# Optimization experiments

Hardware: AMD Instinct MI355X
Metric: run time of the kernel (lower is better)

Reference implementation:

```python
import jax, jax.numpy as jnp
import numpy as np

# SMPL-like kinematic tree parents for 21 body joints (child j -> parent index in the 22-slot feature)
KTREE_PARENTS = jnp.array([0, 0, 0, 1, 2, 3, 4, 5, 6, 7, 8, 9, 9, 9, 12, 13, 14, 16, 17, 18, 19], dtype=jnp.int32)
# np.linspace(22, 64, 3, endpoint=False, dtype=int)[::-1] for num_tokens=64, token_size_div=3, num_joints+1=22
UP_SIZES = [50, 36, 22]
NUM_JOINTS_P1 = 22


def conv1d_rep(x, w, b):
    # x: (B, Cin, L), w: (Cout, Cin, 3), replicate padding of 1 on each side
    xp = jnp.pad(x, ((0, 0), (0, 0), (1, 1)), mode='edge')
    y = jax.lax.conv_general_dilated(xp, w, (1,), 'VALID', dimension_numbers=('NCH', 'OIH', 'NCH'))
    return y + b[None, :, None]


def interp_linear(x, out_size):
    # torch nn.Upsample(mode='linear', align_corners=False) semantics; x: (B, C, L)
    L = x.shape[-1]
    coords = (jnp.arange(out_size, dtype=x.dtype) + 0.5) * (L / out_size) - 0.5
    coords = jnp.clip(coords, 0.0, L - 1)
    lo = jnp.floor(coords).astype(jnp.int32)
    hi = jnp.minimum(lo + 1, L - 1)
    w = coords - lo.astype(x.dtype)
    return x[..., lo] * (1.0 - w) + x[..., hi] * w


def rotation_6d_to_matrix(d6):
    # pytorch3d convention: rows b1, b2, b3 stacked at dim=-2
    a1, a2 = d6[..., :3], d6[..., 3:]
    b1 = a1 / jnp.linalg.norm(a1, axis=-1, keepdims=True)
    a2p = a2 - jnp.sum(b1 * a2, axis=-1, keepdims=True) * b1
    b2 = a2p / jnp.linalg.norm(a2p, axis=-1, keepdims=True)
    b3 = jnp.cross(b1, b2)
    return jnp.stack([b1, b2, b3], axis=-2)


def setup_inputs() -> dict:
    key = jax.random.key(0)
    ks = jax.random.split(key, 8)
    B, T, C, W, J, D = 1024, 64, 512, 512, 21, 6
    s = 0.02
    f32 = jnp.float32
    return {
        'x': jax.random.normal(ks[0], (B, T, C), f32),
        'conv1_w': jax.random.normal(ks[1], (W, C, 3), f32) * s,
        'conv1_b': jnp.zeros((W,), f32),
        'tok_w': jax.random.normal(ks[2], (T, T), f32) * s,
        'tok_b': jnp.zeros((T,), f32),
        'up_w': jax.random.normal(ks[3], (3, W, W, 3), f32) * s,
        'up_b': jnp.zeros((3, W), f32),
        'ln_g': jnp.ones((W,), f32),
        'ln_b': jnp.zeros((W,), f32),
        'beta_w': jax.random.normal(ks[4], (W, 10), f32) * s,
        'beta_b': jnp.zeros((10,), f32),
        'pw1': jax.random.normal(ks[5], (J, 2 * W, W), f32) * s,
        'pb1': jnp.zeros((J, W), f32),
        'pw2': jax.random.normal(ks[6], (J, W, D), f32) * s,
        'pb2': jax.random.normal(ks[7], (J, D), f32) * 0.1,
    }


def reference(x, conv1_w, conv1_b, tok_w, tok_b, up_w, up_b, ln_g, ln_b,
              beta_w, beta_b, pw1, pb1, pw2, pb2):
    # ---- decoder ----
    h = x.transpose(0, 2, 1)                                   # (B, C, T)
    h = jax.nn.relu(conv1d_rep(h, conv1_w, conv1_b))            # (B, W, T)
    # Conv1d(T, T, 1) applied on token axis (after permutes) == matmul over tokens
    h = jax.nn.relu(jnp.einsum('st,bwt->bws', tok_w, h) + tok_b[None, None, :])  # (B, W, T)
    for i, sz in enumerate(UP_SIZES):
        h = conv1d_rep(interp_linear(h, sz), up_w[i], up_b[i])
        if sz != NUM_JOINTS_P1:
            h = jax.nn.relu(h)
    # h: (B, W, 22)
    m = h.mean(axis=-1)                                         # (B, W)
    mu = m.mean(-1, keepdims=True)
    var = m.var(-1, keepdims=True)
    pred_beta = ((m - mu) / jnp.sqrt(var + 1e-5) * ln_g + ln_b) @ beta_w + beta_b  # (B, 10)
    jf = h.transpose(0, 2, 1)                                   # (B, 22, W)
    curr = jf[:, 1:, :]                                         # joint j+1 feats, (B, 21, W)
    parent = jf[:, KTREE_PARENTS, :]                            # parent feats,   (B, 21, W)
    feat = jnp.concatenate([curr, parent], axis=-1)             # (B, 21, 2W)
    hid = jax.nn.relu(jnp.einsum('bjc,jch->bjh', feat, pw1) + pb1[None])
    pose6d = jnp.einsum('bjh,jhd->bjd', hid, pw2) + pb2[None]   # (B, 21, 6)
    rotmat = rotation_6d_to_matrix(pose6d)                      # (B, 21, 3, 3)
    return pose6d, rotmat, pred_beta
```

## Files before the change

### kernel.cpp

```cpp
#include <hip/hip_runtime.h>


typedef unsigned short u16;
typedef unsigned short u16x4 __attribute__((ext_vector_type(4)));
typedef unsigned short u16x8 __attribute__((ext_vector_type(8)));
typedef float f32x4 __attribute__((ext_vector_type(4)));
typedef __bf16 bf16x8 __attribute__((ext_vector_type(8)));

__constant__ int KPAR_C[21] = {0,0,0,1,2,3,4,5,6,7,8,9,9,9,12,13,14,16,17,18,19};

__device__ __forceinline__ u16 bf16rne(float v) {
  unsigned b = __builtin_bit_cast(unsigned, v);
  return (u16)((b + 0x7fffu + ((b >> 16) & 1u)) >> 16);
}
__device__ __forceinline__ float bf16tof(u16 h) {
  unsigned b = ((unsigned)h) << 16;
  return __builtin_bit_cast(float, b);
}
__device__ __forceinline__ f32x4 mfma16(u16x8 a, u16x8 b, f32x4 c) {
  return __builtin_amdgcn_mfma_f32_16x16x32_bf16(
      __builtin_bit_cast(bf16x8, a), __builtin_bit_cast(bf16x8, b), c, 0, 0, 0);
}
__device__ __forceinline__ int unpack_c(int p) {
  return (p & ~31) | (((p >> 3) & 3) << 2) | (p & 3) | ((p & 4) << 2);
}
__device__ __forceinline__ void gload_lds16(const void* g, void* l) {
  __builtin_amdgcn_global_load_lds((const __attribute__((address_space(1))) void*)g,
                                   (__attribute__((address_space(3))) void*)l, 16, 0, 0);
}

__global__ __launch_bounds__(256)
void kwprep(const float* __restrict__ conv1_w, const float* __restrict__ up_w,
            const float* __restrict__ tok_w, u16* __restrict__ WF, u16* __restrict__ TWF) {
  int idx = blockIdx.x * 256 + threadIdx.x;
  if (idx < 786432) {
    const int lane = idx & 63;
    int r = idx >> 6;
    const int nf = r & 15; r >>= 4;
    const int ks = r % 48; r /= 48;
    const int p = r & 1; r >>= 1;
    const int nh = r & 1;
    const int L = r >> 1;
    const float* Wsrc = (L == 0) ? conv1_w : (up_w + (size_t)(L - 1) * 786432);
    const int wcol = unpack_c(nh * 256 + nf * 16 + (lane & 15));
    u16x8 o;
#pragma unroll
    for (int e = 0; e < 8; ++e) {
      const int k = ks * 32 + ((lane >> 4) << 2) + (e & 3) + ((e >> 2) << 4);
      const int c = k & 511, kk = k >> 9;
      const float v = Wsrc[(size_t)wcol * 1536 + c * 3 + kk];
      const u16 h = bf16rne(v);
      o[e] = p ? bf16rne(v - bf16tof(h)) : h;
    }
    *(u16x8*)(WF + (size_t)idx * 8) = o;
  } else if (idx < 786432 + 1024) {
    const int i2 = idx - 786432;
    const int lane = i2 & 63;
    const int r = i2 >> 6;
    const int mf = r & 3;
    const int ks = (r >> 2) & 1;
    const int p = r >> 3;
    const int s = mf * 16 + (lane & 15);
    u16x8 o;
#pragma unroll
    for (int e = 0; e < 8; ++e) {
      const int t = ks * 32 + ((lane >> 4) << 2) + (e & 3) + ((e >> 2) << 4);
      const float v = tok_w[s * 64 + t];
      const u16 h = bf16rne(v);
      o[e] = p ? bf16rne(v - bf16tof(h)) : h;
    }
    *(u16x8*)(TWF + (size_t)i2 * 8) = o;
  }
}

__global__ __launch_bounds__(256)
void kpw1prep(const float* __restrict__ pw1, u16* __restrict__ PWF) {
  const int idx = blockIdx.x * 256 + threadIdx.x;
  if (idx >= 2752512) return;
  const int lane = idx & 63;
  const int nf = (idx >> 6) & 15;
  const int ks = (idx >> 10) & 31;
  const int p = (idx >> 15) & 1;
  const int nh = (idx >> 16) & 1;
  const int j = idx >> 17;
  const int w = unpack_c(nh * 256 + nf * 16 + (lane & 15));
  u16x8 o;
#pragma unroll
  for (int e = 0; e < 8; ++e) {
    const int k = ks * 32 + ((lane >> 4) << 2) + (e & 3) + ((e >> 2) << 4);
    const float v = pw1[((size_t)j * 1024 + k) * 512 + w];
    const u16 h = bf16rne(v);
    o[e] = p ? bf16rne(v - bf16tof(h)) : h;
  }
  *(u16x8*)(PWF + (size_t)idx * 8) = o;
}

template <int SLOT, int ROWS, bool SRCF32, bool F32OUT, bool RELU>
__global__ __launch_bounds__(512, 2)
void conv_gemm(const float* __restrict__ xf,
               const u16* __restrict__ ghi, const u16* __restrict__ glo,
               const u16* __restrict__ wl,
               const float* __restrict__ bias,
               u16* __restrict__ ohi, u16* __restrict__ olo,
               float* __restrict__ of32) {
  constexpr int MFW = SLOT / 16;
  constexpr int SP = (ROWS + 2 + 3) & ~3;
  constexpr int ACH = 32 * SP;
  constexpr int AIT = (ACH + 511) / 512;
  __shared__ u16x8 Ald[2][ACH];
  __shared__ u16x8 Bld[2][2][16][64];

  const int tid = threadIdx.x, lane = tid & 63, w = tid >> 6;
  const int mw = w & 3, nw = w >> 2;
  const int bid = blockIdx.x;
  const int nh = (bid >> 3) & 1;
  const int bg = ((bid >> 4) << 3) | (bid & 7);
  const int bb0 = bg * 4;

  f32x4 acc[MFW][8];
#pragma unroll
  for (int m = 0; m < MFW; ++m)
#pragma unroll
    for (int n = 0; n < 8; ++n) acc[m][n] = (f32x4){0.f, 0.f, 0.f, 0.f};

  auto ASTAGE = [&](int cs1, int dst) {
#pragma unroll
    for (int it = 0; it < AIT; ++it) {
      const int base = it * 512 + w * 64;
      if (base < ACH) {
        const int f = base + lane;
        if constexpr (SRCF32) {
          const int pc = f & 7;
          const int s = (f >> 3) % SP;
          const int b = (f >> 3) / SP;
          int row = s - 1;
          row = row < 0 ? 0 : (row > ROWS - 1 ? ROWS - 1 : row);
          const int q = pc ^ (s & 7);
          const float* src = xf + ((size_t)(bb0 + b) * ROWS + row) * 512 + cs1 * 32 +
                             ((q >> 1) << 2) + ((q & 1) << 4);
          gload_lds16(src, (u16*)&Ald[dst][0] + (size_t)base * 8);
        } else {
          const int pc = f & 3;
          const int sb = f >> 2;
          const int s = sb % SP;
          const int pb = sb / SP;
          int row = s - 1;
          row = row < 0 ? 0 : (row > ROWS - 1 ? ROWS - 1 : row);
          const int q = pc ^ ((s >> 1) & 3);
          const u16* pl = (pb >> 2) ? glo : ghi;
          const u16* src = pl + ((size_t)(bb0 + (pb & 3)) * ROWS + row) * 512 +
                           cs1 * 32 + q * 8;
          gload_lds16(src, (u16*)&Ald[dst][0] + (size_t)base * 8);
        }
      }
    }
  };
  auto BSTAGE = [&](int u2, int nb) {
    const int ks2 = (u2 % 3) * 16 + (u2 / 3);
#pragma unroll
    for (int ci = 0; ci < 4; ++ci) {
      const int cch = w + ci * 8;
      const int p = cch >> 4, nf = cch & 15;
      gload_lds16(wl + ((size_t)(((nh * 2 + p) * 48 + ks2) * 16 + nf)) * 512 + lane * 8,
                  &Bld[nb][p][nf][0]);
    }
  };

  ASTAGE(0, 0);
  BSTAGE(0, 0);
  __syncthreads();

  const int q = lane >> 4;
  for (int cs = 0; cs < 16; ++cs) {
    const int ab = cs & 1;
#pragma unroll
    for (int kk = 0; kk < 3; ++kk) {
      const int u = cs * 3 + kk;
      if (u < 47) BSTAGE(u + 1, (u + 1) & 1);
      if (kk == 0 && cs < 15) ASTAGE(cs + 1, ab ^ 1);
      u16x8 ah[MFW], al[MFW];
#pragma unroll
      for (int m = 0; m < MFW; ++m) {
        const int t = m * 16 + (lane & 15);
        int s = t + kk;
        if (s > ROWS + 1) s = ROWS + 1;
        if constexpr (SRCF32) {
          const int f8 = s & 7;
          const f32x4 va = *(const f32x4*)&Ald[ab][(mw * SP + s) * 8 + ((2 * q) ^ f8)];
          const f32x4 vb = *(const f32x4*)&Ald[ab][(mw * SP + s) * 8 + ((2 * q + 1) ^ f8)];
          const float vv[8] = {va[0], va[1], va[2], va[3], vb[0], vb[1], vb[2], vb[3]};
#pragma unroll
          for (int e = 0; e < 8; ++e) {
            const u16 h = bf16rne(vv[e]);
            ah[m][e] = h;
            al[m][e] = bf16rne(vv[e] - bf16tof(h));
          }
        } else {
          const int pc = q ^ ((s >> 1) & 3);
          ah[m] = Ald[ab][((0 + mw) * SP + s) * 4 + pc];
          al[m] = Ald[ab][((4 + mw) * SP + s) * 4 + pc];
        }
      }
      const int bbuf = u & 1;
      __builtin_amdgcn_s_setprio(1);
#pragma unroll
      for (int n = 0; n < 8; ++n) {
        const u16x8 bh = Bld[bbuf][0][nw * 8 + n][lane];
        const u16x8 bl = Bld[bbuf][1][nw * 8 + n][lane];
#pragma unroll
        for (int m = 0; m < MFW; ++m) {
          acc[m][n] = mfma16(ah[m], bh, acc[m][n]);
          acc[m][n] = mfma16(ah[m], bl, acc[m][n]);
          acc[m][n] = mfma16(al[m], bh, acc[m][n]);
        }
      }
      __builtin_amdgcn_s_setprio(0);
      __syncthreads();
    }
  }

  const int b = bb0 + mw;
#pragma unroll
  for (int m = 0; m < MFW; ++m) {
#pragma unroll
    for (int n = 0; n < 8; ++n) {
      const int col = nh * 256 + nw * 128 + n * 16 + (lane & 15);
      const float bs = bias[unpack_c(col)];
#pragma unroll
      for (int r = 0; r < 4; ++r) {
        const int t = m * 16 + ((lane >> 4) << 2) + r;
        if (t < ROWS) {
          float v = acc[m][n][r] + bs;
          if (RELU) v = fmaxf(v, 0.f);
          const size_t o = ((size_t)b * ROWS + t) * 512 + col;
          if constexpr (F32OUT) {
            of32[o] = v;
          } else {
            const u16 h = bf16rne(v);
            ohi[o] = h;
            olo[o] = bf16rne(v - bf16tof(h));
          }
        }
      }
    }
  }
}

__global__ __launch_bounds__(512, 2)
void tok_mix(const u16* __restrict__ h1hi, const u16* __restrict__ h1lo,
             const u16* __restrict__ twf, const float* __restrict__ tok_b,
             u16* __restrict__ g1hi, u16* __restrict__ g1lo) {
  __shared__ float h1f[64][258];
  __shared__ u16x8 twl[2][2][4][64];
  __shared__ float tbl[64];
  const int tid = threadIdx.x, lane = tid & 63, w = tid >> 6;
  const int mw = w & 3, nw = w >> 2;
  const int b = blockIdx.y, ch = blockIdx.x;

  for (int i = tid; i < 1024; i += 512) ((u16x8*)twl)[i] = ((const u16x8*)twf)[i];
  if (tid < 64) tbl[tid] = tok_b[tid];
  for (int i = tid; i < 2048; i += 512) {
    const int t = i >> 5, c8 = (i & 31) * 8;
    const size_t o = ((size_t)b * 64 + t) * 512 + ch * 256 + c8;
    const u16x8 hv = *(const u16x8*)(h1hi + o);
    const u16x8 lv = *(const u16x8*)(h1lo + o);
#pragma unroll
    for (int e = 0; e < 8; ++e) h1f[t][c8 + e] = bf16tof(hv[e]) + bf16tof(lv[e]);
  }
  __syncthreads();

  f32x4 acc2[8];
#pragma unroll
  for (int n = 0; n < 8; ++n) acc2[n] = (f32x4){0.f, 0.f, 0.f, 0.f};
#pragma unroll
  for (int ksI = 0; ksI < 2; ++ksI) {
    const u16x8 ah = twl[0][ksI][mw][lane];
    const u16x8 al = twl[1][ksI][mw][lane];
    const int t0 = ksI * 32 + ((lane >> 4) << 2);
#pragma unroll
    for (int n = 0; n < 8; ++n) {
      const int c = nw * 128 + n * 16 + (lane & 15);
      u16x8 bh, bl;
#pragma unroll
      for (int e = 0; e < 8; ++e) {
        const float v = h1f[t0 + (e & 3) + ((e >> 2) << 4)][c];
        const u16 h = bf16rne(v);
        bh[e] = h;
        bl[e] = bf16rne(v - bf16tof(h));
      }
      acc2[n] = mfma16(ah, bh, acc2[n]);
      acc2[n] = mfma16(ah, bl, acc2[n]);
      acc2[n] = mfma16(al, bh, acc2[n]);
    }
  }
  __syncthreads();
#pragma unroll
  for (int n = 0; n < 8; ++n) {
    const int c = nw * 128 + n * 16 + (lane & 15);
#pragma unroll
    for (int r = 0; r < 4; ++r) {
      const int s = mw * 16 + ((lane >> 4) << 2) + r;
      h1f[s][c] = fmaxf(acc2[n][r] + tbl[s], 0.f);
    }
  }
  __syncthreads();
  const float scale = (float)(64.0 / 50.0);
  for (int i = tid; i < 50 * 256; i += 512) {
    const int s = i >> 8, c = i & 255;
    float coords = fminf(fmaxf(((float)s + 0.5f) * scale - 0.5f, 0.f), 63.f);
    const int lo = (int)floorf(coords);
    const int hi = lo + 1 < 64 ? lo + 1 : 63;
    const float wv = coords - (float)lo;
    const float v = h1f[lo][c] * (1.f - wv) + h1f[hi][c] * wv;
    const u16 h = bf16rne(v);
    const size_t o = ((size_t)b * 50 + s) * 512 + ch * 256 + c;
    g1hi[o] = h;
    g1lo[o] = bf16rne(v - bf16tof(h));
  }
}

template <int SOUT, int SIN>
__global__ __launch_bounds__(256)
void ginterp(const u16* __restrict__ ahi, const u16* __restrict__ alo,
             u16* __restrict__ ghi, u16* __restrict__ glo) {
  const int idx = blockIdx.x * 256 + threadIdx.x;
  if (idx >= 1024 * SOUT * 64) return;
  const int ch = (idx & 63) * 8;
  const int s = (idx >> 6) % SOUT;
  const int b = (idx >> 6) / SOUT;
  const float scale = (float)((double)SIN / (double)SOUT);
  float coords = fminf(fmaxf(((float)s + 0.5f) * scale - 0.5f, 0.f), (float)(SIN - 1));
  const int lo = (int)floorf(coords);
  const int hi = lo + 1 < SIN ? lo + 1 : SIN - 1;
  const float wv = coords - (float)lo;
  const size_t olo_ = ((size_t)b * SIN + lo) * 512 + ch;
  const size_t ohi_ = ((size_t)b * SIN + hi) * 512 + ch;
  const u16x8 vh0 = *(const u16x8*)(ahi + olo_), vl0 = *(const u16x8*)(alo + olo_);
  const u16x8 vh1 = *(const u16x8*)(ahi + ohi_), vl1 = *(const u16x8*)(alo + ohi_);
  u16x8 oh, ol;
#pragma unroll
  for (int e = 0; e < 8; ++e) {
    const float v0 = bf16tof(vh0[e]) + bf16tof(vl0[e]);
    const float v1 = bf16tof(vh1[e]) + bf16tof(vl1[e]);
    const float v = v0 * (1.f - wv) + v1 * wv;
    const u16 h = bf16rne(v);
    oh[e] = h;
    ol[e] = bf16rne(v - bf16tof(h));
  }
  const size_t oo = ((size_t)b * SOUT + s) * 512 + ch;
  *(u16x8*)(ghi + oo) = oh;
  *(u16x8*)(glo + oo) = ol;
}

__global__ __launch_bounds__(256)
void k_beta(const float* __restrict__ h, const float* __restrict__ ln_g,
            const float* __restrict__ ln_b, const float* __restrict__ beta_w,
            const float* __restrict__ beta_b, float* __restrict__ out) {
  __shared__ float nbuf[512];
  __shared__ float red[32];
  __shared__ float part[160];
  const int tid = threadIdx.x;
  const int b = blockIdx.x;
  const float* hb = h + (size_t)b * (22 * 512);
  float m0 = 0.f, m1 = 0.f;
  for (int t = 0; t < 22; ++t) {
    m0 += hb[t * 512 + tid];
    m1 += hb[t * 512 + tid + 256];
  }
  m0 *= (1.f / 22.f);
  m1 *= (1.f / 22.f);
  float s = m0 + m1, sq = m0 * m0 + m1 * m1;
  for (int off = 32; off > 0; off >>= 1) {
    s += __shfl_down(s, off);
    sq += __shfl_down(sq, off);
  }
  const int lane = tid & 63, wid = tid >> 6;
  if (lane == 0) { red[wid] = s; red[8 + wid] = sq; }
  __syncthreads();
  if (tid == 0) {
    float S = red[0] + red[1] + red[2] + red[3];
    float Q = red[8] + red[9] + red[10] + red[11];
    float mu = S * (1.f / 512.f);
    float var = Q * (1.f / 512.f) - mu * mu;
    red[16] = mu;
    red[17] = 1.f / sqrtf(var + 1e-5f);
  }
  __syncthreads();
  const float mu = red[16], rs = red[17];
  const int uc = unpack_c(tid);
  nbuf[tid] = (m0 - mu) * rs * ln_g[uc] + ln_b[uc];
  nbuf[tid + 256] = (m1 - mu) * rs * ln_g[uc + 256] + ln_b[uc + 256];
  __syncthreads();
  if (tid < 160) {
    const int o = tid >> 4, l = tid & 15;
    float p = 0.f;
    for (int w = l; w < 512; w += 16) p += nbuf[w] * beta_w[unpack_c(w) * 10 + o];
    part[tid] = p;
  }
  __syncthreads();
  if (tid < 10) {
    float p = beta_b[tid];
#pragma unroll
    for (int l = 0; l < 16; ++l) p += part[tid * 16 + l];
    out[(size_t)b * 10 + tid] = p;
  }
}

__global__ __launch_bounds__(512, 2)
void k_pose1(const float* __restrict__ hf, const u16* __restrict__ PWF,
             const float* __restrict__ pb1,
             u16* __restrict__ hidhi, u16* __restrict__ hidlo) {
  __shared__ u16x8 Ald[2][2][8][64];
  __shared__ u16x8 Bld[2][2][16][64];
  const int tid = threadIdx.x, lane = tid & 63, w = tid >> 6;
  const int mw = w & 1, nw = w >> 1;
  const int mb = blockIdx.x & 7, nh = blockIdx.x >> 3;
  const int j = blockIdx.y;
  const int bb0 = mb * 128;
  const int par = KPAR_C[j];
  const size_t pwbase = (size_t)(j * 2 + nh) * 524288;

  f32x4 acc[4][4];
#pragma unroll
  for (int m = 0; m < 4; ++m)
#pragma unroll
    for (int n = 0; n < 4; ++n) acc[m][n] = (f32x4){0.f, 0.f, 0.f, 0.f};

  float4 sF0, sF1;

  auto STAGE = [&](int ks, int nb) {
#pragma unroll
    for (int t = 0; t < 4; ++t) {
      const int cc = t * 8 + w;
      const int p = cc >> 4, nf = cc & 15;
      gload_lds16(PWF + pwbase + ((size_t)(p * 32 + ks) * 16 + nf) * 512 + lane * 8,
                  &Bld[nb][p][nf][0]);
    }
  };
  auto LOADSA = [&](int ks) {
    const int row = (ks < 16) ? (j + 1) : par;
    const int b = bb0 + w * 16 + (lane & 15);
    const int pc0 = (ks & 15) * 32 + ((lane >> 4) << 3);
    const float* src = hf + ((size_t)b * 22 + row) * 512 + pc0;
    sF0 = *(const float4*)src;
    sF1 = *(const float4*)(src + 4);
  };
  auto WRITESA = [&](int nb) {
    float vv[8] = {sF0.x, sF0.y, sF0.z, sF0.w, sF1.x, sF1.y, sF1.z, sF1.w};
    u16x8 hv, lv;
#pragma unroll
    for (int e = 0; e < 8; ++e) {
      const u16 h = bf16rne(vv[e]);
      hv[e] = h;
      lv[e] = bf16rne(vv[e] - bf16tof(h));
    }
    Ald[nb][0][w][lane] = hv;
    Ald[nb][1][w][lane] = lv;
  };

  STAGE(0, 0);
  LOADSA(0);
  WRITESA(0);
  __syncthreads();

  for (int ks = 0; ks < 32; ++ks) {
    const int buf = ks & 1;
    if (ks < 31) { STAGE(ks + 1, buf ^ 1); LOADSA(ks + 1); }
    u16x8 ah[4], al[4], bh[4], bl[4];
#pragma unroll
    for (int m = 0; m < 4; ++m) {
      ah[m] = Ald[buf][0][mw * 4 + m][lane];
      al[m] = Ald[buf][1][mw * 4 + m][lane];
    }
#pragma unroll
    for (int n = 0; n < 4; ++n) {
      bh[n] = Bld[buf][0][nw * 4 + n][lane];
      bl[n] = Bld[buf][1][nw * 4 + n][lane];
    }
    __builtin_amdgcn_s_setprio(1);
#pragma unroll
    for (int n = 0; n < 4; ++n)
#pragma unroll
      for (int m = 0; m < 4; ++m) {
        acc[m][n] = mfma16(ah[m], bh[n], acc[m][n]);
        acc[m][n] = mfma16(ah[m], bl[n], acc[m][n]);
        acc[m][n] = mfma16(al[m], bh[n], acc[m][n]);
      }
    __builtin_amdgcn_s_setprio(0);
    if (ks < 31) WRITESA(buf ^ 1);
    __syncthreads();
  }

#pragma unroll
  for (int m = 0; m < 4; ++m) {
#pragma unroll
    for (int n = 0; n < 4; ++n) {
      const int col = nh * 256 + nw * 64 + n * 16 + (lane & 15);
      const float bs = pb1[(size_t)j * 512 + unpack_c(col)];
#pragma unroll
      for (int r = 0; r < 4; ++r) {
        const int b = bb0 + mw * 64 + m * 16 + ((lane >> 4) << 2) + r;
        float v = fmaxf(acc[m][n][r] + bs, 0.f);
        const size_t o = ((size_t)j * 1024 + b) * 512 + col;
        const u16 h = bf16rne(v);
        hidhi[o] = h;
        hidlo[o] = bf16rne(v - bf16tof(h));
      }
    }
  }
}

__global__ __launch_bounds__(256)
void k_pose2(const u16* __restrict__ hidhi, const u16* __restrict__ hidlo,
             const float* __restrict__ pw2, const float* __restrict__ pb2,
             float* __restrict__ out) {
  __shared__ float w2l[3072];
  __shared__ float part[128 * 12];
  const int tid = threadIdx.x;
  const int mb = blockIdx.x, j = blockIdx.y;
  const int bb0 = mb * 128;
  for (int i = tid; i < 3072; i += 256) {
    const int p = i / 6, d = i - p * 6;
    w2l[i] = pw2[(size_t)j * 3072 + unpack_c(p) * 6 + d];
  }
  __syncthreads();

  const int r = tid >> 1, half = tid & 1;
  const int row = bb0 + r;
  const u16* ph = hidhi + ((size_t)j * 1024 + row) * 512 + half * 256;
  const u16* pl = hidlo + ((size_t)j * 1024 + row) * 512 + half * 256;
  float s[6] = {0.f, 0.f, 0.f, 0.f, 0.f, 0.f};
  for (int c = 0; c < 32; ++c) {
    const u16x8 hv = ((const u16x8*)ph)[c];
    const u16x8 lv = ((const u16x8*)pl)[c];
#pragma unroll
    for (int e = 0; e < 8; ++e) {
      const float v = bf16tof(hv[e]) + bf16tof(lv[e]);
      const int hidx = half * 256 + c * 8 + e;
#pragma unroll
      for (int d = 0; d < 6; ++d) s[d] = fmaf(v, w2l[hidx * 6 + d], s[d]);
    }
  }
#pragma unroll
  for (int d = 0; d < 6; ++d) part[r * 12 + half * 6 + d] = s[d];
  __syncthreads();

  if (tid < 128) {
    const int row2 = bb0 + tid;
    float p6[6];
#pragma unroll
    for (int d = 0; d < 6; ++d)
      p6[d] = part[tid * 12 + d] + part[tid * 12 + 6 + d] + pb2[j * 6 + d];
    float* po = out + ((size_t)row2 * 21 + j) * 6;
#pragma unroll
    for (int d = 0; d < 6; ++d) po[d] = p6[d];
    const float a1x = p6[0], a1y = p6[1], a1z = p6[2];
    const float a2x = p6[3], a2y = p6[4], a2z = p6[5];
    const float inv1 = 1.f / sqrtf(a1x * a1x + a1y * a1y + a1z * a1z);
    const float b1x = a1x * inv1, b1y = a1y * inv1, b1z = a1z * inv1;
    const float dot = b1x * a2x + b1y * a2y + b1z * a2z;
    const float px = a2x - dot * b1x, py = a2y - dot * b1y, pz = a2z - dot * b1z;
    const float inv2 = 1.f / sqrtf(px * px + py * py + pz * pz);
    const float b2x = px * inv2, b2y = py * inv2, b2z = pz * inv2;
    const float b3x = b1y * b2z - b1z * b2y;
    const float b3y = b1z * b2x - b1x * b2z;
    const float b3z = b1x * b2y - b1y * b2x;
    float* ro = out + 129024 + ((size_t)row2 * 21 + j) * 9;
    ro[0] = b1x; ro[1] = b1y; ro[2] = b1z;
    ro[3] = b2x; ro[4] = b2y; ro[5] = b2z;
    ro[6] = b3x; ro[7] = b3y; ro[8] = b3z;
  }
}

extern "C" void kernel_launch(void* const* d_in, const int* in_sizes, int n_in,
                              void* d_out, int out_size, void* d_ws, size_t ws_size,
                              hipStream_t stream) {
  (void)in_sizes; (void)n_in; (void)out_size; (void)ws_size;
  const float* x       = (const float*)d_in[0];
  const float* conv1_w = (const float*)d_in[1];
  const float* conv1_b = (const float*)d_in[2];
  const float* tok_w   = (const float*)d_in[3];
  const float* tok_b   = (const float*)d_in[4];
  const float* up_w    = (const float*)d_in[5];
  const float* up_b    = (const float*)d_in[6];
  const float* ln_g    = (const float*)d_in[7];
  const float* ln_b    = (const float*)d_in[8];
  const float* beta_w  = (const float*)d_in[9];
  const float* beta_b  = (const float*)d_in[10];
  const float* pw1     = (const float*)d_in[11];
  const float* pb1     = (const float*)d_in[12];
  const float* pw2     = (const float*)d_in[13];
  const float* pb2     = (const float*)d_in[14];
  float* outp = (float*)d_out;

  char* base = (char*)d_ws;
  u16* WF  = (u16*)base;
  u16* TWF = WF + 6291456;
  u16* PA16 = (u16*)(base + 12599296);
  u16* PB16 = (u16*)(base + 12599296 + 134217728);
  u16* h1hi = PA16;            u16* h1lo = PA16 + 33554432;
  u16* a2hi = PA16;            u16* a2lo = PA16 + 26214400;
  u16* a3hi = PA16;            u16* a3lo = PA16 + 18874368;
  float* hf = (float*)PA16;
  u16* g1hi = PB16;            u16* g1lo = PB16 + 26214400;
  u16* g2hi = PB16;            u16* g2lo = PB16 + 18874368;
  u16* g3hi = PB16;            u16* g3lo = PB16 + 11534336;
  u16* PWF   = PB16;
  u16* hidhi = PB16 + 22020096;
  u16* hidlo = PB16 + 33030144;

  const size_t WL = 1572864;

  kwprep<<<3076, 256, 0, stream>>>(conv1_w, up_w, tok_w, WF, TWF);
  conv_gemm<64, 64, true, false, true><<<512, 512, 0, stream>>>(
      x, nullptr, nullptr, WF, conv1_b, h1hi, h1lo, nullptr);
  tok_mix<<<dim3(2, 1024), 512, 0, stream>>>(h1hi, h1lo, TWF, tok_b, g1hi, g1lo);
  conv_gemm<64, 50, false, false, true><<<512, 512, 0, stream>>>(
      nullptr, g1hi, g1lo, WF + WL, up_b, a2hi, a2lo, nullptr);
  ginterp<36, 50><<<9216, 256, 0, stream>>>(a2hi, a2lo, g2hi, g2lo);
  conv_gemm<48, 36, false, false, true><<<512, 512, 0, stream>>>(
      nullptr, g2hi, g2lo, WF + 2 * WL, up_b + 512, a3hi, a3lo, nullptr);
  ginterp<22, 36><<<5632, 256, 0, stream>>>(a3hi, a3lo, g3hi, g3lo);
  conv_gemm<32, 22, false, true, false><<<512, 512, 0, stream>>>(
      nullptr, g3hi, g3lo, WF + 3 * WL, up_b + 1024, nullptr, nullptr, hf);
  kpw1prep<<<10752, 256, 0, stream>>>(pw1, PWF);
  k_pose1<<<dim3(16, 21), 512, 0, stream>>>(hf, PWF, pb1, hidhi, hidlo);
  k_beta<<<1024, 256, 0, stream>>>(hf, ln_g, ln_b, beta_w, beta_b, outp + 322560);
  k_pose2<<<dim3(8, 21), 256, 0, stream>>>(hidhi, hidlo, pw2, pb2, outp);
}
```

Baseline: 1.328 ms.

## Restructure conv GEMM pipeline with triple-buffered B and single-buffered A

Replaces the double-buffered A/B LDS staging in the conv GEMM with a single A buffer and a three-deep B ring indexed by kernel tap. Explicit vmcnt waits and raw barriers replace the per-step __syncthreads. A is reloaded after all fragment reads for the last tap, which frees LDS and could raise occupancy. The B weight layout index changes to (kk, cs) ordering, so it must match how the weights are packed, and the hand-counted vmcnt values are fragile.

Result: faster. 1.279 ms (-3.7%).

```diff
diff --git a/kernel.cpp b/kernel.cpp
--- a/kernel.cpp
+++ b/kernel.cpp
@@ -104,11 +104,12 @@
                u16* __restrict__ ohi, u16* __restrict__ olo,
                float* __restrict__ of32) {
   constexpr int MFW = SLOT / 16;
-  constexpr int SP = (ROWS + 2 + 3) & ~3;
-  constexpr int ACH = 32 * SP;
-  constexpr int AIT = (ACH + 511) / 512;
-  __shared__ u16x8 Ald[2][ACH];
-  __shared__ u16x8 Bld[2][2][16][64];
+  constexpr int SP = ROWS + 2;
+  constexpr int AWSP = SRCF32 ? (((SP * 8 + 127) / 128) * 128)
+                              : (((SP * 4 + 63) / 64) * 64);
+  constexpr int ACH = SRCF32 ? 4 * AWSP : 8 * AWSP;
+  __shared__ u16x8 Ald[ACH];
+  __shared__ u16x8 Bld[3][2][16][64];
 
   const int tid = threadIdx.x, lane = tid & 63, w = tid >> 6;
   const int mw = w & 3, nw = w >> 2;
@@ -123,71 +124,72 @@
 #pragma unroll
     for (int n = 0; n < 8; ++n) acc[m][n] = (f32x4){0.f, 0.f, 0.f, 0.f};
 
-  auto ASTAGE = [&](int cs1, int dst) {
-#pragma unroll
-    for (int it = 0; it < AIT; ++it) {
-      const int base = it * 512 + w * 64;
-      if (base < ACH) {
-        const int f = base + lane;
-        if constexpr (SRCF32) {
-          const int pc = f & 7;
-          const int s = (f >> 3) % SP;
-          const int b = (f >> 3) / SP;
-          int row = s - 1;
-          row = row < 0 ? 0 : (row > ROWS - 1 ? ROWS - 1 : row);
-          const int q = pc ^ (s & 7);
-          const float* src = xf + ((size_t)(bb0 + b) * ROWS + row) * 512 + cs1 * 32 +
-                             ((q >> 1) << 2) + ((q & 1) << 4);
-          gload_lds16(src, (u16*)&Ald[dst][0] + (size_t)base * 8);
-        } else {
-          const int pc = f & 3;
-          const int sb = f >> 2;
-          const int s = sb % SP;
-          const int pb = sb / SP;
-          int row = s - 1;
-          row = row < 0 ? 0 : (row > ROWS - 1 ? ROWS - 1 : row);
-          const int q = pc ^ ((s >> 1) & 3);
-          const u16* pl = (pb >> 2) ? glo : ghi;
-          const u16* src = pl + ((size_t)(bb0 + (pb & 3)) * ROWS + row) * 512 +
-                           cs1 * 32 + q * 8;
-          gload_lds16(src, (u16*)&Ald[dst][0] + (size_t)base * 8);
-        }
+  auto ASTAGE = [&](int cs1) {
+    if constexpr (SRCF32) {
+      const int bA = w >> 1;
+      const int h64 = (w & 1) << 6;
+      const float* rowbase = xf + (size_t)(bb0 + bA) * ROWS * 512 + cs1 * 32;
+#pragma unroll
+      for (int it = 0; it < AWSP / 128; ++it) {
+        const int base = it * 128 + h64;
+        const int o = base + lane;
+        int s = o >> 3; s = s > SP - 1 ? SP - 1 : s;
+        const int pc = o & 7;
+        int row = s - 1; row = row < 0 ? 0 : (row > ROWS - 1 ? ROWS - 1 : row);
+        const int q = pc ^ (s & 7);
+        gload_lds16(rowbase + (size_t)row * 512 + ((q >> 1) << 2) + ((q & 1) << 4),
+                    (u16*)Ald + ((size_t)bA * AWSP + base) * 8);
+      }
+    } else {
+      const int bA = w & 3;
+      const u16* pl = (w >= 4) ? glo : ghi;
+      const u16* rowbase = pl + (size_t)(bb0 + bA) * ROWS * 512 + cs1 * 32;
+#pragma unroll
+      for (int it = 0; it < AWSP / 64; ++it) {
+        const int base = it * 64;
+        const int o = base + lane;
+        int s = o >> 2; s = s > SP - 1 ? SP - 1 : s;
+        const int pc = o & 3;
+        int row = s - 1; row = row < 0 ? 0 : (row > ROWS - 1 ? ROWS - 1 : row);
+        const int q = pc ^ ((s >> 1) & 3);
+        gload_lds16(rowbase + (size_t)row * 512 + q * 8,
+                    (u16*)Ald + ((size_t)w * AWSP + base) * 8);
       }
     }
   };
-  auto BSTAGE = [&](int u2, int nb) {
-    const int ks2 = (u2 % 3) * 16 + (u2 / 3);
+  auto BSTAGE = [&](int cs2, int kk2, int buf) {
 #pragma unroll
     for (int ci = 0; ci < 4; ++ci) {
       const int cch = w + ci * 8;
       const int p = cch >> 4, nf = cch & 15;
-      gload_lds16(wl + ((size_t)(((nh * 2 + p) * 48 + ks2) * 16 + nf)) * 512 + lane * 8,
-                  &Bld[nb][p][nf][0]);
+      gload_lds16(wl + ((size_t)(((nh * 2 + p) * 3 + kk2) * 16 + cs2) * 16 + nf) * 512 + lane * 8,
+                  &Bld[buf][p][nf][0]);
     }
   };
 
-  ASTAGE(0, 0);
-  BSTAGE(0, 0);
-  __syncthreads();
+  ASTAGE(0);
+  BSTAGE(0, 0, 0);
+  BSTAGE(0, 1, 1);
 
   const int q = lane >> 4;
   for (int cs = 0; cs < 16; ++cs) {
-    const int ab = cs & 1;
 #pragma unroll
     for (int kk = 0; kk < 3; ++kk) {
-      const int u = cs * 3 + kk;
-      if (u < 47) BSTAGE(u + 1, (u + 1) & 1);
-      if (kk == 0 && cs < 15) ASTAGE(cs + 1, ab ^ 1);
+      if (kk == 2 && cs == 15) {
+        asm volatile("s_waitcnt vmcnt(0)" ::: "memory");
+      } else {
+        asm volatile("s_waitcnt vmcnt(4)" ::: "memory");
+      }
+      __builtin_amdgcn_s_barrier();
       u16x8 ah[MFW], al[MFW];
 #pragma unroll
       for (int m = 0; m < MFW; ++m) {
-        const int t = m * 16 + (lane & 15);
-        int s = t + kk;
-        if (s > ROWS + 1) s = ROWS + 1;
+        int s = m * 16 + (lane & 15) + kk;
+        if (s > SP - 1) s = SP - 1;
         if constexpr (SRCF32) {
           const int f8 = s & 7;
-          const f32x4 va = *(const f32x4*)&Ald[ab][(mw * SP + s) * 8 + ((2 * q) ^ f8)];
-          const f32x4 vb = *(const f32x4*)&Ald[ab][(mw * SP + s) * 8 + ((2 * q + 1) ^ f8)];
+          const f32x4 va = *(const f32x4*)&Ald[(size_t)mw * AWSP + s * 8 + ((2 * q) ^ f8)];
+          const f32x4 vb = *(const f32x4*)&Ald[(size_t)mw * AWSP + s * 8 + ((2 * q + 1) ^ f8)];
           const float vv[8] = {va[0], va[1], va[2], va[3], vb[0], vb[1], vb[2], vb[3]};
 #pragma unroll
           for (int e = 0; e < 8; ++e) {
@@ -197,16 +199,26 @@
           }
         } else {
           const int pc = q ^ ((s >> 1) & 3);
-          ah[m] = Ald[ab][((0 + mw) * SP + s) * 4 + pc];
-          al[m] = Ald[ab][((4 + mw) * SP + s) * 4 + pc];
+          ah[m] = Ald[(size_t)mw * AWSP + s * 4 + pc];
+          al[m] = Ald[(size_t)(4 + mw) * AWSP + s * 4 + pc];
         }
       }
-      const int bbuf = u & 1;
+      asm volatile("s_waitcnt lgkmcnt(0)" ::: "memory");
+      __builtin_amdgcn_sched_barrier(0);
+      if (kk == 2) {
+        __builtin_amdgcn_s_barrier();
+        if (cs < 15) ASTAGE(cs + 1);
+      }
+      {
+        const int nk = (kk + 2) % 3;
+        const int nc = cs + (kk + 2) / 3;
+        if (nc < 16) BSTAGE(nc, nk, nk);
+      }
       __builtin_amdgcn_s_setprio(1);
 #pragma unroll
       for (int n = 0; n < 8; ++n) {
-        const u16x8 bh = Bld[bbuf][0][nw * 8 + n][lane];
-        const u16x8 bl = Bld[bbuf][1][nw * 8 + n][lane];
+        const u16x8 bh = Bld[kk][0][nw * 8 + n][lane];
+        const u16x8 bl = Bld[kk][1][nw * 8 + n][lane];
 #pragma unroll
         for (int m = 0; m < MFW; ++m) {
           acc[m][n] = mfma16(ah[m], bh, acc[m][n]);
@@ -215,7 +227,6 @@
         }
       }
       __builtin_amdgcn_s_setprio(0);
-      __syncthreads();
     }
   }
 
```

## Use chunk-major A tile layout in LDS and split A staging across two steps

Applied to the files above, without the earlier changes.

Changes the shared-memory layout of the A tile from row-major with an XOR swizzle to chunk-major (each 16-byte chunk column laid out contiguously across rows), and drops the row padding. The staging of the next A tile is also split into two halves, issued in the first and second kk sub-steps, so the global-to-LDS loads are spread out instead of bunched into one. This aims to simplify address computation and smooth the load traffic, but the new layout may change LDS bank-conflict behavior on reads.

Measured after the change: 1.301 ms. 1.02x faster.

```diff
diff --git a/kernel.cpp b/kernel.cpp
--- a/kernel.cpp
+++ b/kernel.cpp
@@ -104,10 +104,10 @@
                u16* __restrict__ ohi, u16* __restrict__ olo,
                float* __restrict__ of32) {
   constexpr int MFW = SLOT / 16;
-  constexpr int SP = (ROWS + 2 + 3) & ~3;
-  constexpr int ACH = 32 * SP;
-  constexpr int AIT = (ACH + 511) / 512;
-  __shared__ u16x8 Ald[2][ACH];
+  constexpr int SP = ROWS + 2;
+  constexpr int TOTA = 32 * SP;
+  constexpr int HALF = ((TOTA / 2) + 63) & ~63;
+  __shared__ u16x8 Ald[2][TOTA];
   __shared__ u16x8 Bld[2][2][16][64];
 
   const int tid = threadIdx.x, lane = tid & 63, w = tid >> 6;
@@ -123,71 +123,65 @@
 #pragma unroll
     for (int n = 0; n < 8; ++n) acc[m][n] = (f32x4){0.f, 0.f, 0.f, 0.f};
 
-  auto ASTAGE = [&](int cs1, int dst) {
-#pragma unroll
-    for (int it = 0; it < AIT; ++it) {
+  auto ASTAGE = [&](int cs1, int dst, int LO, int HI) {
+#pragma unroll
+    for (int it = 0; it * 512 < TOTA; ++it) {
       const int base = it * 512 + w * 64;
-      if (base < ACH) {
-        const int f = base + lane;
+      if (base >= LO && base < HI && base < TOTA) {
+        const int c = base + lane;
+        const int s = c % SP;
+        const int g = c / SP;
+        int row = s - 1;
+        row = row < 0 ? 0 : (row > ROWS - 1 ? ROWS - 1 : row);
         if constexpr (SRCF32) {
-          const int pc = f & 7;
-          const int s = (f >> 3) % SP;
-          const int b = (f >> 3) / SP;
-          int row = s - 1;
-          row = row < 0 ? 0 : (row > ROWS - 1 ? ROWS - 1 : row);
-          const int q = pc ^ (s & 7);
-          const float* src = xf + ((size_t)(bb0 + b) * ROWS + row) * 512 + cs1 * 32 +
-                             ((q >> 1) << 2) + ((q & 1) << 4);
+          const int q8 = g & 7, bm = g >> 3;
+          const float* src = xf + ((size_t)(bb0 + bm) * ROWS + row) * 512 +
+                             cs1 * 32 + ((q8 >> 1) << 2) + ((q8 & 1) << 4);
           gload_lds16(src, (u16*)&Ald[dst][0] + (size_t)base * 8);
         } else {
-          const int pc = f & 3;
-          const int sb = f >> 2;
-          const int s = sb % SP;
-          const int pb = sb / SP;
-          int row = s - 1;
-          row = row < 0 ? 0 : (row > ROWS - 1 ? ROWS - 1 : row);
-          const int q = pc ^ ((s >> 1) & 3);
-          const u16* pl = (pb >> 2) ? glo : ghi;
-          const u16* src = pl + ((size_t)(bb0 + (pb & 3)) * ROWS + row) * 512 +
+          const int q = g & 3, bm = (g >> 2) & 3, pl = g >> 4;
+          const u16* srcp = pl ? glo : ghi;
+          const u16* src = srcp + ((size_t)(bb0 + bm) * ROWS + row) * 512 +
                            cs1 * 32 + q * 8;
           gload_lds16(src, (u16*)&Ald[dst][0] + (size_t)base * 8);
         }
       }
     }
   };
-  auto BSTAGE = [&](int u2, int nb) {
-    const int ks2 = (u2 % 3) * 16 + (u2 / 3);
+  auto BSTAGE = [&](int step, int buf) {
+    const int ks2 = (step % 3) * 16 + (step / 3);
 #pragma unroll
     for (int ci = 0; ci < 4; ++ci) {
       const int cch = w + ci * 8;
       const int p = cch >> 4, nf = cch & 15;
       gload_lds16(wl + ((size_t)(((nh * 2 + p) * 48 + ks2) * 16 + nf)) * 512 + lane * 8,
-                  &Bld[nb][p][nf][0]);
+                  &Bld[buf][p][nf][0]);
     }
   };
 
-  ASTAGE(0, 0);
+  ASTAGE(0, 0, 0, TOTA);
   BSTAGE(0, 0);
   __syncthreads();
 
-  const int q = lane >> 4;
+  const int Q = lane >> 4;
   for (int cs = 0; cs < 16; ++cs) {
     const int ab = cs & 1;
 #pragma unroll
     for (int kk = 0; kk < 3; ++kk) {
-      const int u = cs * 3 + kk;
-      if (u < 47) BSTAGE(u + 1, (u + 1) & 1);
-      if (kk == 0 && cs < 15) ASTAGE(cs + 1, ab ^ 1);
+      const int step = cs * 3 + kk;
+      if (step < 47) BSTAGE(step + 1, (step + 1) & 1);
+      if (cs < 15) {
+        if (kk == 0) ASTAGE(cs + 1, ab ^ 1, 0, HALF);
+        if (kk == 1) ASTAGE(cs + 1, ab ^ 1, HALF, TOTA);
+      }
       u16x8 ah[MFW], al[MFW];
 #pragma unroll
       for (int m = 0; m < MFW; ++m) {
-        const int t = m * 16 + (lane & 15);
-        int s = t + kk;
-        if (s > ROWS + 1) s = ROWS + 1;
+        int s = m * 16 + (lane & 15) + kk;
+        if (s > SP - 1) s = SP - 1;
         if constexpr (SRCF32) {
-          const int f8 = s & 7;
-          const f32x4 va = *(const f32x4*)&Ald[ab][(mw * SP + s) * 8 + ((2 * q) ^ f8)];
-          const f32x4 vb = *(const f32x4*)&Ald[ab][(mw * SP + s) * 8 + ((2 * q + 1) ^ f8)];
+          const f32x4 va = *(const f32x4*)&Ald[ab][(mw * 8 + 2 * Q) * SP + s];
+          const f32x4 vb = *(const f32x4*)&Ald[ab][(mw * 8 + 2 * Q + 1) * SP + s];
           const float vv[8] = {va[0], va[1], va[2], va[3], vb[0], vb[1], vb[2], vb[3]};
 #pragma unroll
           for (int e = 0; e < 8; ++e) {
@@ -196,12 +190,11 @@
             al[m][e] = bf16rne(vv[e] - bf16tof(h));
           }
         } else {
-          const int pc = q ^ ((s >> 1) & 3);
-          ah[m] = Ald[ab][((0 + mw) * SP + s) * 4 + pc];
-          al[m] = Ald[ab][((4 + mw) * SP + s) * 4 + pc];
+          ah[m] = Ald[ab][(mw * 4 + Q) * SP + s];
+          al[m] = Ald[ab][((4 + mw) * 4 + Q) * SP + s];
         }
       }
-      const int bbuf = u & 1;
+      const int bbuf = step & 1;
       __builtin_amdgcn_s_setprio(1);
 #pragma unroll
       for (int n = 0; n < 8; ++n) {
```
